# Performance work log

Hardware: AMD Instinct MI355X
Metric: run time of the kernel (lower is better)

The kernel has to match this reference:

```python
import jax, jax.numpy as jnp
import numpy as np

B, T, E, H, D = 2, 2048, 1024, 16, 64
ROPE_BASE = 10000.0


def project(x, k):
    # Lift to Lorentz hyperboloid with curvature magnitude K=exp(k): <lx,lx>_L = -K
    K = jnp.exp(k)
    x0 = jnp.sqrt(K + jnp.sum(x * x, axis=-1, keepdims=True))
    return jnp.concatenate([x0, x], axis=-1)


def layer_norm(x, w, b, eps=1e-5):
    m = jnp.mean(x, axis=-1, keepdims=True)
    v = jnp.mean((x - m) ** 2, axis=-1, keepdims=True)
    return (x - m) * jax.lax.rsqrt(v + eps) * w + b


def setup_inputs() -> dict:
    key = jax.random.key(0)
    ks = jax.random.split(key, 8)
    s = 0.02
    return dict(
        x=jax.random.normal(ks[0], (B, T, E), jnp.float32),
        block_curvature=jnp.asarray(1.0, jnp.float32),
        mlp_curvature=jnp.asarray(1.0, jnp.float32),
        attn_curvatures=jnp.ones((1, H, 1, 1), jnp.float32),
        w_qkv=jax.random.normal(ks[1], (E + 1, 3 * E), jnp.float32) * s,
        w_attn_proj=jax.random.normal(ks[2], ((D + 1) * H, E), jnp.float32) * s,
        b_attn_proj=jnp.zeros((E,), jnp.float32),
        w_mlp_expand=jax.random.normal(ks[3], (E + 1, 4 * E + 3), jnp.float32) * s,
        b_mlp_expand=jnp.zeros((4 * E + 3,), jnp.float32),
        w_mlp_shrink=jax.random.normal(ks[4], (4 * (E + 1), E), jnp.float32) * s,
        b_mlp_shrink=jnp.zeros((E,), jnp.float32),
        ln_w=jnp.ones((E,), jnp.float32),
        ln_b=jnp.zeros((E,), jnp.float32),
    )


def _block(x, block_curvature, mlp_curvature, attn_curvatures, w_qkv,
           w_attn_proj, b_attn_proj, w_mlp_expand, b_mlp_expand,
           w_mlp_shrink, b_mlp_shrink, ln_w, ln_b):
    Bq, Tq = x.shape[0], x.shape[1]
    lx = project(x, block_curvature)  # (B,T,E+1)

    def block_norm(l):
        return project(layer_norm(l[..., 1:], ln_w, ln_b), block_curvature)

    def skip(l, f):  # hyperbolic skip: add space parts, re-lift
        return project(l[..., 1:] + f[..., 1:], block_curvature)

    def attn(l):
        qkv = l @ w_qkv  # (B,T,3E)
        q, k, v = jnp.split(qkv, 3, axis=-1)
        q = q.reshape(Bq, Tq, H, D)
        k = k.reshape(Bq, Tq, H, D)
        v = v.reshape(Bq, Tq, H, D)
        half = D // 2
        inv_freq = 1.0 / (ROPE_BASE ** (jnp.arange(0, D, 2, dtype=jnp.float32) / D))
        freqs = jnp.arange(Tq, dtype=jnp.float32)[:, None] * inv_freq[None, :]
        cos = jnp.cos(freqs)[None, :, None, :]  # (1,T,1,D/2)
        sin = jnp.sin(freqs)[None, :, None, :]

        def rope(t):
            t1, t2 = t[..., :half], t[..., half:]
            return jnp.concatenate([t1 * cos + t2 * sin, -t1 * sin + t2 * cos], axis=-1)

        q = rope(q).transpose(0, 2, 1, 3)  # (B,H,T,D)
        k = rope(k).transpose(0, 2, 1, 3)
        v = v.transpose(0, 2, 1, 3)
        K = jnp.exp(attn_curvatures)  # (1,H,1,1) per-head curvature
        qt = jnp.sqrt(K + jnp.sum(q * q, axis=-1, keepdims=True))  # time coord (B,H,T,1)
        kt = jnp.sqrt(K + jnp.sum(k * k, axis=-1, keepdims=True))
        lv = project(v, attn_curvatures)  # (B,H,T,D+1)
        # Lorentz inner product without materializing (B,H,T,T,D+1)
        inner = jnp.einsum('bhtd,bhsd->bhts', q, k) - qt * jnp.swapaxes(kt, -1, -2)
        ratio = jnp.maximum(-inner / K, 1.0 + 1e-7)
        dis = jnp.sqrt(K) * jnp.arccosh(ratio)  # (B,H,T,T)
        causal = jnp.tril(jnp.ones((Tq, Tq), dtype=bool))
        w = jnp.where(causal, -dis, -jnp.inf)  # neg_dis attention weight + causal bias
        aw = jax.nn.softmax(w, axis=-1)
        o = jnp.einsum('bhts,bhse->bhte', aw, lv)  # (B,H,T,D+1)
        lnorm2 = o[..., :1] ** 2 - jnp.sum(o[..., 1:] ** 2, axis=-1, keepdims=True)
        hn = jnp.sqrt(jnp.maximum(lnorm2, 1e-12))  # Lorentz norm
        o = o * jnp.sqrt(K) / hn  # renormalize back onto hyperboloid
        o = o.transpose(0, 2, 1, 3).reshape(Bq, Tq, H * (D + 1))
        return project(o @ w_attn_proj + b_attn_proj, block_curvature)

    def mlp(l):
        h = project(l @ w_mlp_expand + b_mlp_expand, mlp_curvature)[..., 1:]  # (B,T,4E+3)
        h = jax.nn.gelu(h, approximate=False)
        h = project(h, mlp_curvature)  # (B,T,4(E+1))
        return project(h @ w_mlp_shrink + b_mlp_shrink, block_curvature)

    lx = skip(lx, attn(block_norm(lx)))
    lx = skip(lx, mlp(block_norm(lx)))
    return lx


def reference(x, block_curvature, mlp_curvature, attn_curvatures, w_qkv,
              w_attn_proj, b_attn_proj, w_mlp_expand, b_mlp_expand,
              w_mlp_shrink, b_mlp_shrink, ln_w, ln_b):
    return _block(x, block_curvature, mlp_curvature, attn_curvatures, w_qkv,
                  w_attn_proj, b_attn_proj, w_mlp_expand, b_mlp_expand,
                  w_mlp_shrink, b_mlp_shrink, ln_w, ln_b)
```

## Files before the change

### kernel.cpp

```cpp
#include <hip/hip_runtime.h>
#include <math.h>

#define MM   4096
#define TT   2048
#define HH   16

typedef __bf16 bf16x8 __attribute__((ext_vector_type(8)));
typedef float f32x4 __attribute__((ext_vector_type(4)));

__device__ __forceinline__ void g2l16(const void* g, void* l) {
    __builtin_amdgcn_global_load_lds(
        (__attribute__((address_space(1))) void*)g,
        (__attribute__((address_space(3))) void*)l, 16, 0, 0);
}

#if __has_builtin(__builtin_amdgcn_exp2f)
__device__ __forceinline__ float fexp2(float x) { return __builtin_amdgcn_exp2f(x); }
#else
__device__ __forceinline__ float fexp2(float x) { return exp2f(x); }
#endif
#if __has_builtin(__builtin_amdgcn_logf)
__device__ __forceinline__ float flog2(float x) { return __builtin_amdgcn_logf(x); }
#else
__device__ __forceinline__ float flog2(float x) { return log2f(x); }
#endif
#if __has_builtin(__builtin_amdgcn_sqrtf)
__device__ __forceinline__ float fsqrt_(float x) { return __builtin_amdgcn_sqrtf(x); }
#else
__device__ __forceinline__ float fsqrt_(float x) { return sqrtf(x); }
#endif
#if __has_builtin(__builtin_amdgcn_rcpf)
__device__ __forceinline__ float frcp_(float x) { return __builtin_amdgcn_rcpf(x); }
#else
__device__ __forceinline__ float frcp_(float x) { return 1.0f / x; }
#endif
#if __has_builtin(__builtin_amdgcn_rsqf)
__device__ __forceinline__ float frsq_(float x) { return __builtin_amdgcn_rsqf(x); }
#else
__device__ __forceinline__ float frsq_(float x) { return rsqrtf(x); }
#endif

__device__ __forceinline__ float blockSum256(float v, volatile float* sb) {
    int lane = threadIdx.x & 63, w = threadIdx.x >> 6;
#pragma unroll
    for (int o = 32; o; o >>= 1) v += __shfl_xor(v, o);
    if (lane == 0) sb[w] = v;
    __syncthreads();
    v = sb[0] + sb[1] + sb[2] + sb[3];
    __syncthreads();
    return v;
}

__global__ __launch_bounds__(256) void block_norm_bf_k(
    const float* __restrict__ in, int ld,
    __bf16* __restrict__ out, int ldo,
    const float* __restrict__ lw, const float* __restrict__ lb,
    const float* __restrict__ curv)
{
    int row = blockIdx.x;
    const float* x = in + (size_t)row * ld;
    __bf16* o = out + (size_t)row * ldo;
    __shared__ float sb[4];
    int tid = threadIdx.x;
    float v[4]; float s1 = 0.f, s2 = 0.f;
#pragma unroll
    for (int r = 0; r < 4; r++) {
        float t = x[tid + 256 * r];
        v[r] = t; s1 += t; s2 += t * t;
    }
    s1 = blockSum256(s1, sb);
    s2 = blockSum256(s2, sb);
    float mean = s1 * (1.f / 1024.f);
    float var  = s2 * (1.f / 1024.f) - mean * mean;
    float rs = rsqrtf(var + 1e-5f);
    float y[4]; float ssq = 0.f;
#pragma unroll
    for (int r = 0; r < 4; r++) {
        int i = tid + 256 * r;
        float t = (v[r] - mean) * rs * lw[i] + lb[i];
        y[r] = t; ssq += t * t;
    }
    ssq = blockSum256(ssq, sb);
#pragma unroll
    for (int r = 0; r < 4; r++) o[1 + tid + 256 * r] = (__bf16)y[r];
    if (tid == 0) o[0] = (__bf16)sqrtf(expf(*curv) + ssq);
    if (tid < ldo - 1025) o[1025 + tid] = (__bf16)0.f;
}

__global__ __launch_bounds__(256) void row_x0_k(
    float* __restrict__ buf, int stride, int n, const float* __restrict__ curv)
{
    int row = blockIdx.x;
    float* base = buf + (size_t)row * stride;
    __shared__ float sb[4];
    float s = 0.f;
    for (int i = threadIdx.x; i < n; i += 256) { float t = base[1 + i]; s += t * t; }
    s = blockSum256(s, sb);
    if (threadIdx.x == 0) base[0] = sqrtf(expf(*curv) + s);
}

__global__ __launch_bounds__(256) void row_x0_tail_k(
    __bf16* __restrict__ h,
    const __bf16* __restrict__ ln,
    const __bf16* __restrict__ Bt,
    const float* __restrict__ bias,
    const float* __restrict__ curv)
{
    int row = blockIdx.x;
    __bf16* base = h + (size_t)row * 4224;
    const __bf16* lnr = ln + (size_t)row * 1088;
    const __bf16* B0 = Bt + (size_t)4096 * 1088;
    const __bf16* B1 = Bt + (size_t)4097 * 1088;
    const __bf16* B2 = Bt + (size_t)4098 * 1088;
    __shared__ float sb[4];
    float d0 = 0.f, d1 = 0.f, d2 = 0.f;
    for (int i = threadIdx.x; i < 1088; i += 256) {
        float a = (float)lnr[i];
        d0 += a * (float)B0[i];
        d1 += a * (float)B1[i];
        d2 += a * (float)B2[i];
    }
    d0 = blockSum256(d0, sb);
    d1 = blockSum256(d1, sb);
    d2 = blockSum256(d2, sb);
    float t3[3] = {d0 + bias[4096], d1 + bias[4097], d2 + bias[4098]};
    float ssq_t = 0.f;
#pragma unroll
    for (int j = 0; j < 3; j++) {
        float v = t3[j];
        v = 0.5f * v * (1.f + erff(v * 0.70710678118654752f));
        t3[j] = v; ssq_t += v * v;
    }
    if (threadIdx.x == 0) {
        base[1 + 4096] = (__bf16)t3[0];
        base[1 + 4097] = (__bf16)t3[1];
        base[1 + 4098] = (__bf16)t3[2];
    }
    float s = 0.f;
    for (int i = threadIdx.x; i < 4096; i += 256) { float t = (float)base[1 + i]; s += t * t; }
    s = blockSum256(s, sb) + ssq_t;
    if (threadIdx.x == 0) base[0] = (__bf16)sqrtf(expf(*curv) + s);
    if (threadIdx.x < 124) base[4100 + threadIdx.x] = (__bf16)0.f;
}

__global__ __launch_bounds__(256) void wt_k(
    const float* __restrict__ W, int K, int N,
    __bf16* __restrict__ Wt, int Kp)
{
    __shared__ float s[32][33];
    int tx = threadIdx.x & 31, ty = threadIdx.x >> 5;
    int k0 = blockIdx.x * 32, n0 = blockIdx.y * 32;
#pragma unroll
    for (int r = 0; r < 4; r++) {
        int k = k0 + ty + 8 * r, n = n0 + tx;
        s[ty + 8 * r][tx] = (k < K && n < N) ? W[(size_t)k * N + n] : 0.f;
    }
    __syncthreads();
#pragma unroll
    for (int r = 0; r < 4; r++) {
        int n = n0 + ty + 8 * r, k = k0 + tx;
        if (n < N) Wt[(size_t)n * Kp + k] = (__bf16)s[tx][ty + 8 * r];
    }
}

template<bool BIAS, bool GELU, bool OUTBF>
__global__ __launch_bounds__(512, 2) void mgemm256_k(
    const __bf16* __restrict__ A, int lda,
    const __bf16* __restrict__ Bt, int ldb, int NB,
    const float* __restrict__ bias,
    void* __restrict__ Cout, int ldc,
    int N, int Kp)
{
    __shared__ __bf16 sAB[65536];
    const int tid = threadIdx.x;
    const int w = tid >> 6, lane = tid & 63;
    const int wm = w >> 2, wn = w & 3;
    const int lr = lane & 15, lq = lane >> 4;
    const int m0 = blockIdx.y * 256, n0 = blockIdx.x * 256;

    const int rr  = tid >> 3;
    const int csw = ((tid & 7) ^ (rr & 7)) << 3;
    const __bf16* gA[4]; const __bf16* gB[4];
#pragma unroll
    for (int c = 0; c < 4; c++) {
        gA[c] = A + (size_t)(m0 + c * 64 + rr) * lda + csw;
        int rb = n0 + c * 64 + rr; rb = (rb < NB) ? rb : (NB - 1);
        gB[c] = Bt + (size_t)rb * ldb + csw;
    }
    __bf16* lA = sAB + (w << 9);
    __bf16* lB = sAB + 32768 + (w << 9);

    const int off0 = (lq * 8) ^ ((lr & 7) << 3);
    const int off1 = off0 ^ 32;
    const int arow = wm * 128 + lr;
    const int brow = wn * 64 + lr;

    f32x4 zero = {0.f, 0.f, 0.f, 0.f};
    f32x4 acc[8][4];
#pragma unroll
    for (int i = 0; i < 8; i++)
#pragma unroll
        for (int j = 0; j < 4; j++) acc[i][j] = zero;

#pragma unroll
    for (int c = 0; c < 4; c++) {
        g2l16(gA[c], lA + c * 4096);
        g2l16(gB[c], lB + c * 4096);
    }
    asm volatile("s_waitcnt vmcnt(0)" ::: "memory");
    __builtin_amdgcn_s_barrier();

    const int NT = Kp >> 6;
    for (int kt = 0; kt < NT; ++kt) {
        const int cur = kt & 1;
        const __bf16* pA = sAB + cur * 16384;
        const __bf16* pB = sAB + 32768 + cur * 16384;
        bf16x8 af[4][2], bfr[4][2];

        if (kt + 1 < NT) {
            const int ko = (kt + 1) << 6;
            __bf16* dA = lA + (cur ^ 1) * 16384;
            __bf16* dB = lB + (cur ^ 1) * 16384;
#pragma unroll
            for (int c = 0; c < 4; c++) {
                g2l16(gA[c] + ko, dA + c * 4096);
                g2l16(gB[c] + ko, dB + c * 4096);
            }
        }
#pragma unroll
        for (int i = 0; i < 4; i++) {
            const __bf16* r = pA + (arow + i * 16) * 64;
            af[i][0] = *(const bf16x8*)(r + off0);
            af[i][1] = *(const bf16x8*)(r + off1);
        }
#pragma unroll
        for (int j = 0; j < 2; j++) {
            const __bf16* r = pB + (brow + j * 16) * 64;
            bfr[j][0] = *(const bf16x8*)(r + off0);
            bfr[j][1] = *(const bf16x8*)(r + off1);
        }
        __builtin_amdgcn_s_barrier();
        __builtin_amdgcn_s_setprio(1);
#pragma unroll
        for (int ks = 0; ks < 2; ks++)
#pragma unroll
            for (int i = 0; i < 4; i++)
#pragma unroll
                for (int j = 0; j < 2; j++)
                    acc[i][j] = __builtin_amdgcn_mfma_f32_16x16x32_bf16(af[i][ks], bfr[j][ks], acc[i][j], 0, 0, 0);
        __builtin_amdgcn_s_setprio(0);
        __builtin_amdgcn_s_barrier();

#pragma unroll
        for (int j = 2; j < 4; j++) {
            const __bf16* r = pB + (brow + j * 16) * 64;
            bfr[j][0] = *(const bf16x8*)(r + off0);
            bfr[j][1] = *(const bf16x8*)(r + off1);
        }
        __builtin_amdgcn_s_barrier();
        __builtin_amdgcn_s_setprio(1);
#pragma unroll
        for (int ks = 0; ks < 2; ks++)
#pragma unroll
            for (int i = 0; i < 4; i++)
#pragma unroll
                for (int j = 2; j < 4; j++)
                    acc[i][j] = __builtin_amdgcn_mfma_f32_16x16x32_bf16(af[i][ks], bfr[j][ks], acc[i][j], 0, 0, 0);
        __builtin_amdgcn_s_setprio(0);
        __builtin_amdgcn_s_barrier();

#pragma unroll
        for (int i = 0; i < 4; i++) {
            const __bf16* r = pA + (arow + 64 + i * 16) * 64;
            af[i][0] = *(const bf16x8*)(r + off0);
            af[i][1] = *(const bf16x8*)(r + off1);
        }
        __builtin_amdgcn_s_barrier();
        __builtin_amdgcn_s_setprio(1);
#pragma unroll
        for (int ks = 0; ks < 2; ks++)
#pragma unroll
            for (int i = 0; i < 4; i++)
#pragma unroll
                for (int j = 0; j < 2; j++)
                    acc[4 + i][j] = __builtin_amdgcn_mfma_f32_16x16x32_bf16(af[i][ks], bfr[j][ks], acc[4 + i][j], 0, 0, 0);
        __builtin_amdgcn_s_setprio(0);
        __builtin_amdgcn_s_barrier();

        __builtin_amdgcn_s_setprio(1);
#pragma unroll
        for (int ks = 0; ks < 2; ks++)
#pragma unroll
            for (int i = 0; i < 4; i++)
#pragma unroll
                for (int j = 2; j < 4; j++)
                    acc[4 + i][j] = __builtin_amdgcn_mfma_f32_16x16x32_bf16(af[i][ks], bfr[j][ks], acc[4 + i][j], 0, 0, 0);
        __builtin_amdgcn_s_setprio(0);
        asm volatile("s_waitcnt vmcnt(0) lgkmcnt(0)" ::: "memory");
        __builtin_amdgcn_s_barrier();
    }

#pragma unroll
    for (int j = 0; j < 4; j++) {
        const int n = n0 + wn * 64 + j * 16 + lr;
        if (n < N) {
            const float bv = BIAS ? bias[n] : 0.f;
#pragma unroll
            for (int i = 0; i < 8; i++) {
#pragma unroll
                for (int r = 0; r < 4; r++) {
                    const int m = m0 + wm * 128 + i * 16 + lq * 4 + r;
                    float v = acc[i][j][r] + bv;
                    if (GELU) v = 0.5f * v * (1.f + erff(v * 0.70710678118654752f));
                    if (OUTBF) ((__bf16*)Cout)[(size_t)m * ldc + n] = (__bf16)v;
                    else       ((float*)Cout)[(size_t)m * ldc + n] = v;
                }
            }
        }
    }
}

template<bool BIAS, bool GELU, bool SKIP>
__global__ __launch_bounds__(256) void mgemm64_k(
    const __bf16* __restrict__ A, int lda,
    const __bf16* __restrict__ Bt, int ldb,
    const float* __restrict__ bias,
    const float* __restrict__ skip, int ldskip,
    float* __restrict__ Cout, int ldc,
    int N, int Kp)
{
    __shared__ __bf16 sA[128 * 32];
    __shared__ __bf16 sB[64 * 32];
    int tid = threadIdx.x;
    int w = tid >> 6, lane = tid & 63;
    int m0 = blockIdx.y * 128, n0 = blockIdx.x * 64;
    const __bf16* Ab = A + (size_t)m0 * lda;
    const __bf16* Bb = Bt + (size_t)n0 * ldb;

    f32x4 zero = {0.f, 0.f, 0.f, 0.f};
    f32x4 acc[4][2];
#pragma unroll
    for (int i = 0; i < 4; i++) { acc[i][0] = zero; acc[i][1] = zero; }

    int mw = (w & 1) * 64, nw = (w >> 1) * 32;
    int lr = lane & 15, lq = lane >> 4;
    int fko = lq * 8;

    int rA = tid >> 2, kkA = (tid & 3) * 8;
    __bf16* lA1 = &sA[(size_t)(w * 64) * 8];
    __bf16* lA2 = &sA[(size_t)(256 + w * 64) * 8];
    __bf16* lB  = &sB[(size_t)(w * 64) * 8];

    for (int k0 = 0; k0 < Kp; k0 += 32) {
        g2l16(Ab + (size_t)rA * lda + k0 + kkA, lA1);
        g2l16(Ab + (size_t)(rA + 64) * lda + k0 + kkA, lA2);
        g2l16(Bb + (size_t)rA * ldb + k0 + kkA, lB);
        __syncthreads();
        bf16x8 af[4], bf[2];
#pragma unroll
        for (int i = 0; i < 4; i++) af[i] = *(const bf16x8*)&sA[(mw + i * 16 + lr) * 32 + fko];
#pragma unroll
        for (int j = 0; j < 2; j++) bf[j] = *(const bf16x8*)&sB[(nw + j * 16 + lr) * 32 + fko];
#pragma unroll
        for (int i = 0; i < 4; i++)
#pragma unroll
            for (int j = 0; j < 2; j++)
                acc[i][j] = __builtin_amdgcn_mfma_f32_16x16x32_bf16(af[i], bf[j], acc[i][j], 0, 0, 0);
        __syncthreads();
    }

#pragma unroll
    for (int j = 0; j < 2; j++) {
        int n = n0 + nw + j * 16 + lr;
        if (n < N) {
            float bv = BIAS ? bias[n] : 0.f;
#pragma unroll
            for (int i = 0; i < 4; i++) {
#pragma unroll
                for (int r = 0; r < 4; r++) {
                    int m = m0 + mw + i * 16 + lq * 4 + r;
                    float v = acc[i][j][r] + bv;
                    if (GELU) v = 0.5f * v * (1.f + erff(v * 0.70710678118654752f));
                    if (SKIP) v += skip[(size_t)m * ldskip + n];
                    Cout[(size_t)m * ldc + n] = v;
                }
            }
        }
    }
}

__global__ __launch_bounds__(256) void rope_k(
    float* __restrict__ QKV, const float* __restrict__ curv,
    float* __restrict__ qt, float* __restrict__ kt,
    __bf16* __restrict__ Kb, __bf16* __restrict__ Obf)
{
    int row = blockIdx.x;
    int b = row >> 11, t = row & (TT - 1);
    int wv = threadIdx.x >> 6, d = threadIdx.x & 63;
    int j = d & 31;
    float fr = (float)t * powf(10000.0f, -(float)(2 * j) / 64.0f);
    float cv = cosf(fr), sv = sinf(fr);
    float sgn = (d < 32) ? sv : -sv;
    for (int h = wv; h < HH; h += 4) {
        float Kh = expf(curv[h]);
        float* base = QKV + (size_t)row * 3072 + h * 64;
        float q = base[d], k = base[1024 + d];
        float qp = __shfl_xor(q, 32);
        float kp = __shfl_xor(k, 32);
        float qr = q * cv + qp * sgn;
        float kr = k * cv + kp * sgn;
        base[d] = qr;
        size_t oidx = ((size_t)(b * HH + h) * TT + t);
        Kb[oidx * 64 + d] = (__bf16)kr;
        float sq = qr * qr, sk = kr * kr;
#pragma unroll
        for (int o = 32; o; o >>= 1) {
            sq += __shfl_xor(sq, o);
            sk += __shfl_xor(sk, o);
        }
        if (d == 0) {
            qt[oidx] = sqrtf(Kh + sq);
            kt[oidx] = sqrtf(Kh + sk);
        }
    }
    if (threadIdx.x < 16) Obf[(size_t)row * 1056 + 1040 + threadIdx.x] = (__bf16)0.f;
}

__global__ __launch_bounds__(256) void vtrans_k(
    const float* __restrict__ QKV, const float* __restrict__ curv,
    __bf16* __restrict__ Vtb, float* __restrict__ vt)
{
    __shared__ float sT[64 * 65];
    int bh = blockIdx.y; int h = bh & (HH - 1); int b = bh >> 4;
    int t0 = blockIdx.x * 64;
    int tid = threadIdx.x, w = tid >> 6, lane = tid & 63;
    float Kh = expf(curv[h]);
    const float* vbase = QKV + (size_t)(b * TT + t0) * 3072 + 2048 + h * 64;
#pragma unroll 4
    for (int i = 0; i < 16; i++) {
        int tr = w * 16 + i;
        float v = vbase[(size_t)tr * 3072 + lane];
        sT[lane * 65 + tr] = v;
        float s = v * v;
#pragma unroll
        for (int o = 32; o; o >>= 1) s += __shfl_xor(s, o);
        if (lane == 0) vt[(size_t)bh * TT + t0 + tr] = sqrtf(Kh + s);
    }
    __syncthreads();
    int d = tid >> 2, seg = tid & 3;
    const float* r = &sT[d * 65 + seg * 16];
    bf16x8 o0, o1;
#pragma unroll
    for (int i = 0; i < 8; i++) { o0[i] = (__bf16)r[i]; o1[i] = (__bf16)r[8 + i]; }
    __bf16* dst = Vtb + ((size_t)bh * 64 + d) * TT + t0 + seg * 16;
    *(bf16x8*)dst = o0;
    *(bf16x8*)(dst + 8) = o1;
}

__global__ __launch_bounds__(256, 4) void flash_k(
    const float* __restrict__ QKV,
    const __bf16* __restrict__ Kb, const __bf16* __restrict__ Vtb,
    const float* __restrict__ qt, const float* __restrict__ kt,
    const float* __restrict__ vt,
    const float* __restrict__ curv,
    __bf16* __restrict__ O)
{
    __shared__ __bf16 sK[4096];
    __shared__ __bf16 sVt[4096];
    __shared__ __bf16 sP[4 * 16 * 72];
    __shared__ float skt[64], svt[64];

    int bh = blockIdx.x; int h = bh & (HH - 1); int b = bh >> 4;
    int pi = blockIdx.y;
    float Kh = expf(curv[h]);
    float sqKh = sqrtf(Kh), msqK = -sqKh, invKh = 1.0f / Kh;
    const float* tok = QKV + (size_t)b * TT * 3072 + h * 64;
    const char* KbB = (const char*)Kb + (size_t)bh * TT * 128;
    const char* VtB = (const char*)Vtb + (size_t)bh * 64 * (TT * 2);
    const float* qtp = qt + (size_t)bh * TT;
    const float* ktp = kt + (size_t)bh * TT;
    const float* vtp = vt + (size_t)bh * TT;

    int tid = threadIdx.x;
    int w = tid >> 6, lane = tid & 63;
    int m = lane & 15, quad = lane >> 4;
    int qA = pi * 32, qB = (63 - pi) * 32;
    int myBase = (w < 2) ? (qA + 16 * w) : (qB + 16 * (w - 2));
    int myJmax = (myBase + 15) >> 6;
    int blockJmax = (qB + 31) >> 6;
    __bf16* sPw = &sP[w * 16 * 72];

    bf16x8 qhi[2], qlo[2];
    {
        const float* qrow = tok + (size_t)(myBase + m) * 3072;
#pragma unroll
        for (int ks = 0; ks < 2; ks++) {
            const float* s = qrow + quad * 8 + 32 * ks;
            float4 f0 = *(const float4*)s;
            float4 f1 = *(const float4*)(s + 4);
            float fa[8] = {f0.x, f0.y, f0.z, f0.w, f1.x, f1.y, f1.z, f1.w};
#pragma unroll
            for (int jj = 0; jj < 8; jj++) {
                __bf16 hv = (__bf16)fa[jj];
                qhi[ks][jj] = hv;
                qlo[ks][jj] = (__bf16)(fa[jj] - (float)hv);
            }
        }
    }
    float qtv[4]; int qg[4];
#pragma unroll
    for (int r = 0; r < 4; r++) { qg[r] = myBase + quad * 4 + r; qtv[r] = qtp[qg[r]]; }

    f32x4 zero = {0.f, 0.f, 0.f, 0.f};
    f32x4 accO[4];
#pragma unroll
    for (int nt = 0; nt < 4; nt++) accO[nt] = zero;
    float lsumr[4] = {}, o0r[4] = {};

    char* sKb  = (char*)sK  + w * 1024;
    char* sVb  = (char*)sVt + w * 1024;

    for (int j = 0; j <= blockJmax; ++j) {
        int sb = j << 6;
        __syncthreads();
        {
            const char* kg = KbB + (size_t)(sb + lane) * 128 + w * 16;
            g2l16(kg,      sKb);
            g2l16(kg + 64, sKb + 4096);
            const char* vg = VtB + (size_t)lane * (TT * 2) + sb * 2 + w * 16;
            g2l16(vg,      sVb);
            g2l16(vg + 64, sVb + 4096);
        }
        if (tid < 64) skt[tid] = ktp[sb + tid];
        else if (tid < 128) svt[tid - 64] = vtp[sb + tid - 64];
        __syncthreads();

        if (j > myJmax) continue;

        f32x4 accS[4];
#pragma unroll
        for (int nt = 0; nt < 4; nt++) accS[nt] = zero;
#pragma unroll
        for (int nt = 0; nt < 4; nt++) {
#pragma unroll
            for (int ksp = 0; ksp < 2; ksp++) {
                bf16x8 bk = *(const bf16x8*)&sK[((ksp * 4 + quad) * 64 + nt * 16 + m) * 8];
                accS[nt] = __builtin_amdgcn_mfma_f32_16x16x32_bf16(qhi[ksp], bk, accS[nt], 0, 0, 0);
                accS[nt] = __builtin_amdgcn_mfma_f32_16x16x32_bf16(qlo[ksp], bk, accS[nt], 0, 0, 0);
            }
        }
#pragma unroll
        for (int nt = 0; nt < 4; nt++) {
            int col = nt * 16 + m;
            int sglob = sb + col;
            float ktv = skt[col], vtv = svt[col];
#pragma unroll
            for (int r = 0; r < 4; r++) {
                float dot = accS[nt][r];
                float rdiff = fmaf(qtv[r], ktv, -dot);
                float ratio = fmaxf(rdiff * invKh, 1.0f + 1e-7f);
                float y = ratio + fsqrt_(fmaf(ratio, ratio, -1.0f));
                float pv = fexp2(msqK * flog2(y));
                float p = (sglob <= qg[r]) ? pv : 0.0f;
                lsumr[r] += p;
                o0r[r] = fmaf(p, vtv, o0r[r]);
                sPw[(quad * 4 + r) * 72 + col] = (__bf16)p;
            }
        }
        __asm__ volatile("s_waitcnt lgkmcnt(0)" ::: "memory");
#pragma unroll
        for (int ksp = 0; ksp < 2; ksp++) {
            bf16x8 aP = *(const bf16x8*)&sPw[m * 72 + ksp * 32 + quad * 8];
#pragma unroll
            for (int nt = 0; nt < 4; nt++) {
                bf16x8 bV = *(const bf16x8*)&sVt[((ksp * 4 + quad) * 64 + nt * 16 + m) * 8];
                accO[nt] = __builtin_amdgcn_mfma_f32_16x16x32_bf16(aP, bV, accO[nt], 0, 0, 0);
            }
        }
    }

#pragma unroll
    for (int r = 0; r < 4; r++) {
#pragma unroll
        for (int off = 1; off < 16; off <<= 1) {
            lsumr[r] += __shfl_xor(lsumr[r], off);
            o0r[r]   += __shfl_xor(o0r[r], off);
        }
    }
#pragma unroll
    for (int r = 0; r < 4; r++) {
        float inv = frcp_(lsumr[r]);
        float o0f = o0r[r] * inv;
        float ov[4]; float part = 0.f;
#pragma unroll
        for (int nt = 0; nt < 4; nt++) { float t = accO[nt][r] * inv; ov[nt] = t; part += t * t; }
        part += __shfl_xor(part, 1);
        part += __shfl_xor(part, 2);
        part += __shfl_xor(part, 4);
        part += __shfl_xor(part, 8);
        float scale = sqKh * frsq_(fmaxf(o0f * o0f - part, 1e-12f));
        size_t orow = (size_t)(b * TT + qg[r]) * 1056 + h * 65;
        if (m == 0) O[orow] = (__bf16)(o0f * scale);
#pragma unroll
        for (int nt = 0; nt < 4; nt++) O[orow + 1 + nt * 16 + m] = (__bf16)(ov[nt] * scale);
    }
}

extern "C" void kernel_launch(void* const* d_in, const int* in_sizes, int n_in,
                              void* d_out, int out_size, void* d_ws, size_t ws_size,
                              hipStream_t stream) {
    const float* x    = (const float*)d_in[0];
    const float* bc   = (const float*)d_in[1];
    const float* mc   = (const float*)d_in[2];
    const float* ac   = (const float*)d_in[3];
    const float* w_qkv = (const float*)d_in[4];
    const float* w_ap  = (const float*)d_in[5];
    const float* b_ap  = (const float*)d_in[6];
    const float* w_me  = (const float*)d_in[7];
    const float* b_me  = (const float*)d_in[8];
    const float* w_ms  = (const float*)d_in[9];
    const float* b_ms  = (const float*)d_in[10];
    const float* lnw  = (const float*)d_in[11];
    const float* lnb  = (const float*)d_in[12];
    float* out = (float*)d_out;
    float* ws  = (float*)d_ws;

    float* R      = ws;
    float* qkvbuf = R;
    float* X2     = R;
    __bf16* h_bf  = (__bf16*)(R + 4194304);
    float* p      = R + 12845056;
    __bf16* ln_bf = (__bf16*)p;  p += 2228224;
    __bf16* o_bf  = (__bf16*)p;  p += 2162688;
    __bf16* qkvT  = (__bf16*)p;  p += 1671168;
    __bf16* apT   = (__bf16*)p;  p += 540672;
    float*  meT_f = p;           p += 2229856;
    float*  msT_f = p;           p += 2162688;
    float* Qt = p;               p += 2 * HH * TT;
    float* Kt = p;               p += 2 * HH * TT;
    float* Vt = p;
    __bf16* meT = (__bf16*)meT_f;
    __bf16* msT = (__bf16*)msT_f;
    __bf16* Kb  = (__bf16*)meT_f;
    __bf16* Vtb = (__bf16*)msT_f;

    wt_k<<<dim3(34, 96),  256, 0, stream>>>(w_qkv, 1025, 3072, qkvT, 1088);
    wt_k<<<dim3(33, 32),  256, 0, stream>>>(w_ap,  1040, 1024, apT,  1056);

    block_norm_bf_k<<<MM, 256, 0, stream>>>(x, 1024, ln_bf, 1088, lnw, lnb, bc);
    mgemm256_k<false, false, false><<<dim3(12, 16), 512, 0, stream>>>(
        ln_bf, 1088, qkvT, 1088, 3072, nullptr, qkvbuf, 3072, 3072, 1088);
    rope_k<<<MM, 256, 0, stream>>>(qkvbuf, ac, Qt, Kt, Kb, o_bf);
    vtrans_k<<<dim3(32, 32), 256, 0, stream>>>(qkvbuf, ac, Vtb, Vt);
    flash_k<<<dim3(2 * HH, 32), 256, 0, stream>>>(qkvbuf, Kb, Vtb, Qt, Kt, Vt, ac, o_bf);
    wt_k<<<dim3(34, 129), 256, 0, stream>>>(w_me,  1025, 4099, meT, 1088);
    wt_k<<<dim3(132, 32), 256, 0, stream>>>(w_ms,  4100, 1024, msT, 4224);
    mgemm64_k<true, false, true><<<dim3(16, 32), 256, 0, stream>>>(
        o_bf, 1056, apT, 1056, b_ap, x, 1024, X2, 1024, 1024, 1056);
    block_norm_bf_k<<<MM, 256, 0, stream>>>(X2, 1024, ln_bf, 1088, lnw, lnb, bc);
    mgemm256_k<true, true, true><<<dim3(16, 16), 512, 0, stream>>>(
        ln_bf, 1088, meT, 1088, 4099, b_me, (void*)(h_bf + 1), 4224, 4099, 1088);
    row_x0_tail_k<<<MM, 256, 0, stream>>>(h_bf, ln_bf, meT, b_me, mc);
    mgemm64_k<true, false, true><<<dim3(16, 32), 256, 0, stream>>>(
        h_bf, 4224, msT, 4224, b_ms, X2, 1024, out + 1, 1025, 1024, 4224);
    row_x0_k<<<MM, 256, 0, stream>>>(out, 1025, 1024, bc);
}
```

Before: 511.2 us.

## Replace 128x64 GEMM with double-buffered swizzled 128x128 tile kernel

The two N=1024 GEMMs (attention projection and MLP shrink) move from a 128x64 tile with BK=32 and two barriers per step to a 128x128 tile with BK=64. The new kernel double-buffers LDS via global_load_lds, XOR-swizzles the LDS layout to avoid bank conflicts, and remaps block IDs for L2 locality. To support BK=64 it pads the attention output and transposed proj weights from 1056 to 1088 columns. Each block now carries more accumulator registers, and the grid shrinks to 256 blocks, which may underfill the GPU's compute units.

```diff
diff --git a/kernel.cpp b/kernel.cpp
--- a/kernel.cpp
+++ b/kernel.cpp
@@ -321,7 +321,7 @@
 }
 
 template<bool BIAS, bool GELU, bool SKIP>
-__global__ __launch_bounds__(256) void mgemm64_k(
+__global__ __launch_bounds__(256, 2) void mgemm128_k(
     const __bf16* __restrict__ A, int lda,
     const __bf16* __restrict__ Bt, int ldb,
     const float* __restrict__ bias,
@@ -329,56 +329,119 @@
     float* __restrict__ Cout, int ldc,
     int N, int Kp)
 {
-    __shared__ __bf16 sA[128 * 32];
-    __shared__ __bf16 sB[64 * 32];
-    int tid = threadIdx.x;
-    int w = tid >> 6, lane = tid & 63;
-    int m0 = blockIdx.y * 128, n0 = blockIdx.x * 64;
-    const __bf16* Ab = A + (size_t)m0 * lda;
-    const __bf16* Bb = Bt + (size_t)n0 * ldb;
+    __shared__ __bf16 sAB[32768];
+    const int tid = threadIdx.x;
+    const int w = tid >> 6, lane = tid & 63;
+    const int wm = w >> 1, wn = w & 1;
+    const int lr = lane & 15, lq = lane >> 4;
+
+    const int bid = blockIdx.x;
+    const int cpx = gridDim.x >> 3;
+    const int swz = (bid & 7) * cpx + (bid >> 3);
+    const int m0 = (swz >> 3) * 128, n0 = (swz & 7) * 128;
+
+    const int rr  = tid >> 3;
+    const int csw = ((tid & 7) ^ (rr & 7)) << 3;
+    const __bf16* gA[4]; const __bf16* gB[4];
+#pragma unroll
+    for (int c = 0; c < 4; c++) {
+        gA[c] = A + (size_t)(m0 + c * 32 + rr) * lda + csw;
+        gB[c] = Bt + (size_t)(n0 + c * 32 + rr) * ldb + csw;
+    }
+    __bf16* lA = sAB + (w << 9);
+    __bf16* lB = sAB + 16384 + (w << 9);
+
+    const int off0 = (lq * 8) ^ ((lr & 7) << 3);
+    const int off1 = off0 ^ 32;
+    const int arow = wm * 64 + lr;
+    const int brow = wn * 64 + lr;
 
     f32x4 zero = {0.f, 0.f, 0.f, 0.f};
-    f32x4 acc[4][2];
-#pragma unroll
-    for (int i = 0; i < 4; i++) { acc[i][0] = zero; acc[i][1] = zero; }
-
-    int mw = (w & 1) * 64, nw = (w >> 1) * 32;
-    int lr = lane & 15, lq = lane >> 4;
-    int fko = lq * 8;
-
-    int rA = tid >> 2, kkA = (tid & 3) * 8;
-    __bf16* lA1 = &sA[(size_t)(w * 64) * 8];
-    __bf16* lA2 = &sA[(size_t)(256 + w * 64) * 8];
-    __bf16* lB  = &sB[(size_t)(w * 64) * 8];
-
-    for (int k0 = 0; k0 < Kp; k0 += 32) {
-        g2l16(Ab + (size_t)rA * lda + k0 + kkA, lA1);
-        g2l16(Ab + (size_t)(rA + 64) * lda + k0 + kkA, lA2);
-        g2l16(Bb + (size_t)rA * ldb + k0 + kkA, lB);
-        __syncthreads();
-        bf16x8 af[4], bf[2];
-#pragma unroll
-        for (int i = 0; i < 4; i++) af[i] = *(const bf16x8*)&sA[(mw + i * 16 + lr) * 32 + fko];
-#pragma unroll
-        for (int j = 0; j < 2; j++) bf[j] = *(const bf16x8*)&sB[(nw + j * 16 + lr) * 32 + fko];
-#pragma unroll
-        for (int i = 0; i < 4; i++)
-#pragma unroll
-            for (int j = 0; j < 2; j++)
-                acc[i][j] = __builtin_amdgcn_mfma_f32_16x16x32_bf16(af[i], bf[j], acc[i][j], 0, 0, 0);
-        __syncthreads();
-    }
-
-#pragma unroll
-    for (int j = 0; j < 2; j++) {
-        int n = n0 + nw + j * 16 + lr;
+    f32x4 acc[4][4];
+#pragma unroll
+    for (int i = 0; i < 4; i++)
+#pragma unroll
+        for (int j = 0; j < 4; j++) acc[i][j] = zero;
+
+#pragma unroll
+    for (int c = 0; c < 4; c++) {
+        g2l16(gA[c], lA + c * 2048);
+        g2l16(gB[c], lB + c * 2048);
+    }
+    asm volatile("s_waitcnt vmcnt(0)" ::: "memory");
+    __builtin_amdgcn_s_barrier();
+
+    const int NT = Kp >> 6;
+    for (int kt = 0; kt < NT; ++kt) {
+        const int cur = kt & 1;
+        const __bf16* pA = sAB + cur * 8192;
+        const __bf16* pB = sAB + 16384 + cur * 8192;
+        bf16x8 af[4][2], bfr[4][2];
+
+        if (kt + 1 < NT) {
+            const int ko = (kt + 1) << 6;
+            __bf16* dA = lA + (cur ^ 1) * 8192;
+            __bf16* dB = lB + (cur ^ 1) * 8192;
+#pragma unroll
+            for (int c = 0; c < 4; c++) {
+                g2l16(gA[c] + ko, dA + c * 2048);
+                g2l16(gB[c] + ko, dB + c * 2048);
+            }
+        }
+#pragma unroll
+        for (int i = 0; i < 4; i++) {
+            const __bf16* r = pA + (arow + i * 16) * 64;
+            af[i][0] = *(const bf16x8*)(r + off0);
+            af[i][1] = *(const bf16x8*)(r + off1);
+        }
+#pragma unroll
+        for (int j = 0; j < 2; j++) {
+            const __bf16* r = pB + (brow + j * 16) * 64;
+            bfr[j][0] = *(const bf16x8*)(r + off0);
+            bfr[j][1] = *(const bf16x8*)(r + off1);
+        }
+        __builtin_amdgcn_s_barrier();
+        __builtin_amdgcn_s_setprio(1);
+#pragma unroll
+        for (int ks = 0; ks < 2; ks++)
+#pragma unroll
+            for (int i = 0; i < 4; i++)
+#pragma unroll
+                for (int j = 0; j < 2; j++)
+                    acc[i][j] = __builtin_amdgcn_mfma_f32_16x16x32_bf16(af[i][ks], bfr[j][ks], acc[i][j], 0, 0, 0);
+        __builtin_amdgcn_s_setprio(0);
+        __builtin_amdgcn_s_barrier();
+
+#pragma unroll
+        for (int j = 2; j < 4; j++) {
+            const __bf16* r = pB + (brow + j * 16) * 64;
+            bfr[j][0] = *(const bf16x8*)(r + off0);
+            bfr[j][1] = *(const bf16x8*)(r + off1);
+        }
+        __builtin_amdgcn_s_barrier();
+        __builtin_amdgcn_s_setprio(1);
+#pragma unroll
+        for (int ks = 0; ks < 2; ks++)
+#pragma unroll
+            for (int i = 0; i < 4; i++)
+#pragma unroll
+                for (int j = 2; j < 4; j++)
+                    acc[i][j] = __builtin_amdgcn_mfma_f32_16x16x32_bf16(af[i][ks], bfr[j][ks], acc[i][j], 0, 0, 0);
+        __builtin_amdgcn_s_setprio(0);
+        asm volatile("s_waitcnt vmcnt(0) lgkmcnt(0)" ::: "memory");
+        __builtin_amdgcn_s_barrier();
+    }
+
+#pragma unroll
+    for (int j = 0; j < 4; j++) {
+        const int n = n0 + wn * 64 + j * 16 + lr;
         if (n < N) {
-            float bv = BIAS ? bias[n] : 0.f;
+            const float bv = BIAS ? bias[n] : 0.f;
 #pragma unroll
             for (int i = 0; i < 4; i++) {
 #pragma unroll
                 for (int r = 0; r < 4; r++) {
-                    int m = m0 + mw + i * 16 + lq * 4 + r;
+                    const int m = m0 + wm * 64 + i * 16 + lq * 4 + r;
                     float v = acc[i][j][r] + bv;
                     if (GELU) v = 0.5f * v * (1.f + erff(v * 0.70710678118654752f));
                     if (SKIP) v += skip[(size_t)m * ldskip + n];
@@ -423,7 +486,7 @@
             kt[oidx] = sqrtf(Kh + sk);
         }
     }
-    if (threadIdx.x < 16) Obf[(size_t)row * 1056 + 1040 + threadIdx.x] = (__bf16)0.f;
+    if (threadIdx.x < 48) Obf[(size_t)row * 1088 + 1040 + threadIdx.x] = (__bf16)0.f;
 }
 
 __global__ __launch_bounds__(256) void vtrans_k(
@@ -599,7 +662,7 @@
         part += __shfl_xor(part, 4);
         part += __shfl_xor(part, 8);
         float scale = sqKh * frsq_(fmaxf(o0f * o0f - part, 1e-12f));
-        size_t orow = (size_t)(b * TT + qg[r]) * 1056 + h * 65;
+        size_t orow = (size_t)(b * TT + qg[r]) * 1088 + h * 65;
         if (m == 0) O[orow] = (__bf16)(o0f * scale);
 #pragma unroll
         for (int nt = 0; nt < 4; nt++) O[orow + 1 + nt * 16 + m] = (__bf16)(ov[nt] * scale);
@@ -631,9 +694,9 @@
     __bf16* h_bf  = (__bf16*)(R + 4194304);
     float* p      = R + 12845056;
     __bf16* ln_bf = (__bf16*)p;  p += 2228224;
-    __bf16* o_bf  = (__bf16*)p;  p += 2162688;
+    __bf16* o_bf  = (__bf16*)p;  p += 2228224;
     __bf16* qkvT  = (__bf16*)p;  p += 1671168;
-    __bf16* apT   = (__bf16*)p;  p += 540672;
+    __bf16* apT   = (__bf16*)p;  p += 557056;
     float*  meT_f = p;           p += 2229856;
     float*  msT_f = p;           p += 2162688;
     float* Qt = p;               p += 2 * HH * TT;
@@ -645,7 +708,7 @@
     __bf16* Vtb = (__bf16*)msT_f;
 
     wt_k<<<dim3(34, 96),  256, 0, stream>>>(w_qkv, 1025, 3072, qkvT, 1088);
-    wt_k<<<dim3(33, 32),  256, 0, stream>>>(w_ap,  1040, 1024, apT,  1056);
+    wt_k<<<dim3(34, 32),  256, 0, stream>>>(w_ap,  1040, 1024, apT,  1088);
 
     block_norm_bf_k<<<MM, 256, 0, stream>>>(x, 1024, ln_bf, 1088, lnw, lnb, bc);
     mgemm256_k<false, false, false><<<dim3(12, 16), 512, 0, stream>>>(
@@ -655,13 +718,13 @@
     flash_k<<<dim3(2 * HH, 32), 256, 0, stream>>>(qkvbuf, Kb, Vtb, Qt, Kt, Vt, ac, o_bf);
     wt_k<<<dim3(34, 129), 256, 0, stream>>>(w_me,  1025, 4099, meT, 1088);
     wt_k<<<dim3(132, 32), 256, 0, stream>>>(w_ms,  4100, 1024, msT, 4224);
-    mgemm64_k<true, false, true><<<dim3(16, 32), 256, 0, stream>>>(
-        o_bf, 1056, apT, 1056, b_ap, x, 1024, X2, 1024, 1024, 1056);
+    mgemm128_k<true, false, true><<<dim3(256), 256, 0, stream>>>(
+        o_bf, 1088, apT, 1088, b_ap, x, 1024, X2, 1024, 1024, 1088);
     block_norm_bf_k<<<MM, 256, 0, stream>>>(X2, 1024, ln_bf, 1088, lnw, lnb, bc);
     mgemm256_k<true, true, true><<<dim3(16, 16), 512, 0, stream>>>(
         ln_bf, 1088, meT, 1088, 4099, b_me, (void*)(h_bf + 1), 4224, 4099, 1088);
     row_x0_tail_k<<<MM, 256, 0, stream>>>(h_bf, ln_bf, meT, b_me, mc);
-    mgemm64_k<true, false, true><<<dim3(16, 32), 256, 0, stream>>>(
+    mgemm128_k<true, false, true><<<dim3(256), 256, 0, stream>>>(
         h_bf, 4224, msT, 4224, b_ms, X2, 1024, out + 1, 1025, 1024, 4224);
     row_x0_k<<<MM, 256, 0, stream>>>(out, 1025, 1024, bc);
 }
```

After: 478.2 us. 6.5% less time.
